# Performance work log

Measured on AMD Instinct MI355X. Metric: run time of the kernel, lower is better.

Reference implementation:

```python
import jax, jax.numpy as jnp
import numpy as np

H = 128          # num_hidden
B = 512          # number of graphs (segments)
N0, N1, N2 = 500_000, 500_000, 250_000  # nodes per rank
EPS = 1e-5       # LayerNorm eps (torch default)


def setup_inputs() -> dict:
    key = jax.random.key(0)
    ks = jax.random.split(key, 24)
    s = 0.02
    inp = {
        "h0": jax.random.normal(ks[0], (N0, H), jnp.float32),
        "h1": jax.random.normal(ks[1], (N1, H), jnp.float32),
        "h2": jax.random.normal(ks[2], (N2, H), jnp.float32),
        "b0": jnp.sort(jax.random.randint(ks[3], (N0,), 0, B, jnp.int32)),
        "b1": jnp.sort(jax.random.randint(ks[4], (N1,), 0, B, jnp.int32)),
        "b2": jnp.sort(jax.random.randint(ks[5], (N2,), 0, B, jnp.int32)),
        "Wg0": jax.random.normal(ks[6], (H, 1), jnp.float32) * s,
        "bg0": jnp.zeros((1,), jnp.float32),
        "Wg1": jax.random.normal(ks[7], (H, 1), jnp.float32) * s,
        "bg1": jnp.zeros((1,), jnp.float32),
        "Wg2": jax.random.normal(ks[8], (H, 1), jnp.float32) * s,
        "bg2": jnp.zeros((1,), jnp.float32),
        "Wp0": jax.random.normal(ks[9], (4 * H, H), jnp.float32) * s,
        "bp0": jnp.zeros((H,), jnp.float32),
        "Wp1": jax.random.normal(ks[10], (4 * H, H), jnp.float32) * s,
        "bp1": jnp.zeros((H,), jnp.float32),
        "Wp2": jax.random.normal(ks[11], (4 * H, H), jnp.float32) * s,
        "bp2": jnp.zeros((H,), jnp.float32),
        "gamma": jnp.ones((3 * H,), jnp.float32),
        "beta": jnp.zeros((3 * H,), jnp.float32),
        "W1": jax.random.normal(ks[12], (3 * H, H), jnp.float32) * s,
        "b1f": jnp.zeros((H,), jnp.float32),
        "W2": jax.random.normal(ks[13], (H, 1), jnp.float32) * s,
        "b2f": jnp.zeros((1,), jnp.float32),
    }
    return inp


def _rank_vec(h, b, Wg, bg, Wp, bp):
    # gated multi-aggregation pooling over segments b -> [B, 4H] -> Linear -> [B, H]
    g = jax.nn.sigmoid(h @ Wg + bg)                      # [N, 1]
    sum_p = jax.ops.segment_sum(h, b, num_segments=B)    # [B, H]
    cnt = jax.ops.segment_sum(jnp.ones((h.shape[0], 1), h.dtype), b, num_segments=B)
    mean_p = sum_p / jnp.maximum(cnt, 1.0)
    max_p = jax.ops.segment_max(h, b, num_segments=B)
    max_p = jnp.where(cnt > 0, max_p, 0.0)               # guard empty segments
    gsum_p = jax.ops.segment_sum(g * h, b, num_segments=B)
    agg = jnp.concatenate([sum_p, mean_p, max_p, gsum_p], axis=1)  # [B, 4H]
    return agg @ Wp + bp


def reference(h0, h1, h2, b0, b1, b2,
              Wg0, bg0, Wg1, bg1, Wg2, bg2,
              Wp0, bp0, Wp1, bp1, Wp2, bp2,
              gamma, beta, W1, b1f, W2, b2f):
    r0 = _rank_vec(h0, b0, Wg0, bg0, Wp0, bp0)
    r1 = _rank_vec(h1, b1, Wg1, bg1, Wp1, bp1)
    r2 = _rank_vec(h2, b2, Wg2, bg2, Wp2, bp2)
    state = jnp.concatenate([r0, r1, r2], axis=1)        # [B, 3H]
    mu = jnp.mean(state, axis=-1, keepdims=True)
    var = jnp.mean(jnp.square(state - mu), axis=-1, keepdims=True)
    xn = (state - mu) * jax.lax.rsqrt(var + EPS) * gamma + beta
    x = jax.nn.silu(xn)
    x = jax.nn.silu(x @ W1 + b1f)
    out = x @ W2 + b2f                                   # [B, 1]
    return out[:, 0] if out.shape[-1] == 1 else out
```

## Files before the change

kernel.cpp:

```cpp
#include <hip/hip_runtime.h>
#include <math.h>

constexpr int H  = 128;
constexpr int B  = 512;
constexpr int RANK_STRIDE = 3 * B * H + B;
constexpr int TOTAL_WS    = 3 * RANK_STRIDE;

constexpr int ROWS_PER_WAVE  = 128;
constexpr int ROWS_PER_BLOCK = 4 * ROWS_PER_WAVE;

__device__ __forceinline__ float atomicMaxF(float* addr, float val) {
  if (val >= 0.f) {
    return __int_as_float(atomicMax((int*)addr, __float_as_int(val)));
  } else {
    return __uint_as_float(atomicMin((unsigned int*)addr, __float_as_uint(val)));
  }
}

__global__ __launch_bounds__(256) void init_ws_kernel(float* ws) {
  int i = blockIdx.x * blockDim.x + threadIdx.x;
  if (i >= TOTAL_WS) return;
  int o = i % RANK_STRIDE;
  bool ismax = (o >= 2 * B * H) && (o < 3 * B * H);
  ws[i] = ismax ? __int_as_float(0xFF800000) : 0.0f;
}

template <int CTRL>
__device__ __forceinline__ float dpp_add(float x) {
  int mi = __builtin_amdgcn_update_dpp(0, __float_as_int(x), CTRL, 0xF, 0xF, true);
  return x + __int_as_float(mi);
}

__global__ __launch_bounds__(256) void rank_fused_kernel(
    const float* __restrict__ h0, const int* __restrict__ b0,
    const float* __restrict__ Wg0, const float* __restrict__ bg0, int N0, int nb0,
    const float* __restrict__ h1, const int* __restrict__ b1,
    const float* __restrict__ Wg1, const float* __restrict__ bg1, int N1, int nb1,
    const float* __restrict__ h2, const int* __restrict__ b2,
    const float* __restrict__ Wg2, const float* __restrict__ bg2, int N2,
    float* __restrict__ ws)
{
  const int blk = blockIdx.x;
  const float* h; const int* b; const float* Wg; const float* bg;
  float* base; int N; int lblk;
  if (blk < nb0) {
    h = h0; b = b0; Wg = Wg0; bg = bg0; base = ws;                   N = N0; lblk = blk;
  } else if (blk < nb0 + nb1) {
    h = h1; b = b1; Wg = Wg1; bg = bg1; base = ws + RANK_STRIDE;     N = N1; lblk = blk - nb0;
  } else {
    h = h2; b = b2; Wg = Wg2; bg = bg2; base = ws + 2 * RANK_STRIDE; N = N2; lblk = blk - nb0 - nb1;
  }

  const int lane = threadIdx.x & 63;
  const int wv   = threadIdx.x >> 6;
  const int half = lane >> 5;
  const int c    = lane & 31;

  const int wstart = (lblk * 4 + wv) * ROWS_PER_WAVE;
  if (wstart >= N) return;
  const int wend = min(wstart + ROWS_PER_WAVE, N);

  float* __restrict__ sumb  = base;
  float* __restrict__ gsumb = base + B * H;
  float* __restrict__ maxb  = base + 2 * B * H;
  float* __restrict__ cntb  = base + 3 * B * H;

  const float4 wg  = ((const float4*)Wg)[c];
  const float  bgv = bg[0];

  const int bv0 = b[min(wstart + lane, N - 1)];
  const int bv1 = b[min(wstart + 64 + lane, N - 1)];

  float4 s  = {0.f, 0.f, 0.f, 0.f};
  float4 gq = {0.f, 0.f, 0.f, 0.f};
  float4 m  = {-INFINITY, -INFINITY, -INFINITY, -INFINITY};
  int cnt = 0;
  int cur = -1;

  auto flushLane = [&]() {
    if (cur >= 0) {
      const int bi = cur * H + c * 4;
      atomicAdd(sumb + bi + 0, s.x);  atomicAdd(sumb + bi + 1, s.y);
      atomicAdd(sumb + bi + 2, s.z);  atomicAdd(sumb + bi + 3, s.w);
      atomicAdd(gsumb + bi + 0, gq.x); atomicAdd(gsumb + bi + 1, gq.y);
      atomicAdd(gsumb + bi + 2, gq.z); atomicAdd(gsumb + bi + 3, gq.w);
      atomicMaxF(maxb + bi + 0, m.x); atomicMaxF(maxb + bi + 1, m.y);
      atomicMaxF(maxb + bi + 2, m.z); atomicMaxF(maxb + bi + 3, m.w);
      if (c == 0 && cnt) atomicAdd(cntb + cur, (float)cnt);
      s = {0.f, 0.f, 0.f, 0.f};
      gq = {0.f, 0.f, 0.f, 0.f};
      m = {-INFINITY, -INFINITY, -INFINITY, -INFINITY};
      cnt = 0;
    }
  };

  auto gateOf = [&](float4 v) -> float {
    float p = fmaf(v.x, wg.x, fmaf(v.y, wg.y, fmaf(v.z, wg.z, v.w * wg.w)));
    p = dpp_add<0xB1>(p);
    p = dpp_add<0x4E>(p);
    p = dpp_add<0x124>(p);
    p = dpp_add<0x128>(p);
    p += __int_as_float(__builtin_amdgcn_ds_swizzle(__float_as_int(p), 0x401F));
    return 1.0f / (1.0f + __expf(-(p + bgv)));
  };

  auto accum = [&](float4 v, float gt) {
    s.x += v.x; s.y += v.y; s.z += v.z; s.w += v.w;
    gq.x = fmaf(gt, v.x, gq.x); gq.y = fmaf(gt, v.y, gq.y);
    gq.z = fmaf(gt, v.z, gq.z); gq.w = fmaf(gt, v.w, gq.w);
    m.x = fmaxf(m.x, v.x); m.y = fmaxf(m.y, v.y);
    m.z = fmaxf(m.z, v.z); m.w = fmaxf(m.w, v.w);
  };

  const float4* __restrict__ hp = (const float4*)h;

  auto LOADB = [&](float4* dst, int baseRow) {
    const float4* rp = hp + (size_t)baseRow * 32 + c;
    #pragma unroll
    for (int i = 0; i < 8; ++i) dst[i] = rp[(size_t)(2 * i + half) * 32];
  };

  float4 cbuf[8];
  bool pre = false;

  int r = wstart;
  while (r + 64 <= wend) {
    const int bv = (r - wstart < 64) ? bv0 : bv1;
    const int sA = __shfl(bv, 0);
    const int sB = __shfl(bv, 63);
    if (sA == sB) {
      if (sA != cur) { flushLane(); cur = sA; }
      if (!pre) LOADB(cbuf, r);
      const bool pnext = (r + 128 <= wend);
      float4 nbuf[8];
      #pragma unroll
      for (int g = 0; g < 4; ++g) {
        if (g < 3) {
          LOADB(nbuf, r + (g + 1) * 16);
        } else if (pnext) {
          LOADB(nbuf, r + 64);
        }
        #pragma unroll
        for (int i = 0; i < 8; ++i) {
          const float gt = gateOf(cbuf[i]);
          accum(cbuf[i], gt);
        }
        #pragma unroll
        for (int i = 0; i < 8; ++i) cbuf[i] = nbuf[i];
      }
      pre = pnext;
      cnt += 32;
    } else {
      #pragma unroll 4
      for (int i = 0; i < 32; ++i) {
        const int seg = __shfl(bv, 2 * i + half);
        const float4 v = hp[(size_t)(r + 2 * i + half) * 32 + c];
        const float gt = gateOf(v);
        if (seg != cur) { flushLane(); cur = seg; }
        accum(v, gt);
        ++cnt;
      }
      pre = false;
    }
    r += 64;
  }
  while (r + 2 <= wend) {
    const int o = r - wstart;
    const int bv = (o < 64) ? bv0 : bv1;
    const int seg = __shfl(bv, (o & 63) + half);
    const float4 v = hp[(size_t)(r + half) * 32 + c];
    const float gt = gateOf(v);
    if (seg != cur) { flushLane(); cur = seg; }
    accum(v, gt);
    ++cnt;
    r += 2;
  }
  if (r < wend) {
    const int o = r - wstart;
    const int bv = (o < 64) ? bv0 : bv1;
    const int seg = __shfl(bv, o & 63);
    const float4 v = hp[(size_t)r * 32 + c];
    const float gt = gateOf(v);
    if (half == 0) {
      if (seg != cur) { flushLane(); cur = seg; }
      accum(v, gt);
      ++cnt;
    }
  }

  {
    const int   ocur = __shfl_xor(cur, 32);
    const float osx = __shfl_xor(s.x, 32), osy = __shfl_xor(s.y, 32);
    const float osz = __shfl_xor(s.z, 32), osw = __shfl_xor(s.w, 32);
    const float ogx = __shfl_xor(gq.x, 32), ogy = __shfl_xor(gq.y, 32);
    const float ogz = __shfl_xor(gq.z, 32), ogw = __shfl_xor(gq.w, 32);
    const float omx = __shfl_xor(m.x, 32), omy = __shfl_xor(m.y, 32);
    const float omz = __shfl_xor(m.z, 32), omw = __shfl_xor(m.w, 32);
    const int   ocnt = __shfl_xor(cnt, 32);
    if (ocur == cur && cur >= 0) {
      if (half == 0) {
        s.x += osx; s.y += osy; s.z += osz; s.w += osw;
        gq.x += ogx; gq.y += ogy; gq.z += ogz; gq.w += ogw;
        m.x = fmaxf(m.x, omx); m.y = fmaxf(m.y, omy);
        m.z = fmaxf(m.z, omz); m.w = fmaxf(m.w, omw);
        cnt += ocnt;
      } else {
        cur = -1;
      }
    }
  }
  flushLane();
}

__device__ __forceinline__ float siluf(float x) {
  return x / (1.0f + __expf(-x));
}

__global__ __launch_bounds__(128) void finalize_kernel(
    const float* __restrict__ ws,
    const float* __restrict__ Wp0, const float* __restrict__ bp0,
    const float* __restrict__ Wp1, const float* __restrict__ bp1,
    const float* __restrict__ Wp2, const float* __restrict__ bp2,
    const float* __restrict__ gamma, const float* __restrict__ beta,
    const float* __restrict__ W1, const float* __restrict__ b1f,
    const float* __restrict__ W2, const float* __restrict__ b2f,
    float* __restrict__ out)
{
  __shared__ float aggL[4][4 * H];
  __shared__ float state[4][3 * H];
  __shared__ float red[8];

  const int j = threadIdx.x;
  const int lane = j & 63;
  const int wv = j >> 6;
  const int gbase = blockIdx.x * 4;

  const float* Wp[3] = {Wp0, Wp1, Wp2};
  const float* bp[3] = {bp0, bp1, bp2};

  for (int k = 0; k < 3; ++k) {
    const float* sumb  = ws + k * RANK_STRIDE;
    const float* gsumb = sumb + B * H;
    const float* maxb  = sumb + 2 * B * H;
    const float* cntb  = sumb + 3 * B * H;

    for (int g = 0; g < 4; ++g) {
      const int bidx = gbase + g;
      const float cc = cntb[bidx];
      const float cm = fmaxf(cc, 1.0f);
      const float sv = sumb[bidx * H + j];
      const float mv = maxb[bidx * H + j];
      const float gv = gsumb[bidx * H + j];
      aggL[g][j]         = sv;
      aggL[g][H + j]     = sv / cm;
      aggL[g][2 * H + j] = (cc > 0.f) ? mv : 0.f;
      aggL[g][3 * H + j] = gv;
    }
    __syncthreads();

    const float bpv = bp[k][j];
    float r0 = bpv, r1 = bpv, r2 = bpv, r3 = bpv;
    const float* W = Wp[k];
    for (int i = 0; i < 4 * H; ++i) {
      const float w = W[i * H + j];
      r0 = fmaf(aggL[0][i], w, r0);
      r1 = fmaf(aggL[1][i], w, r1);
      r2 = fmaf(aggL[2][i], w, r2);
      r3 = fmaf(aggL[3][i], w, r3);
    }
    state[0][k * H + j] = r0;
    state[1][k * H + j] = r1;
    state[2][k * H + j] = r2;
    state[3][k * H + j] = r3;
    __syncthreads();
  }

  for (int g = 0; g < 4; ++g) {
    const float v0 = state[g][j];
    const float v1 = state[g][H + j];
    const float v2 = state[g][2 * H + j];
    float ps = v0 + v1 + v2;
    float pq = v0 * v0 + v1 * v1 + v2 * v2;
    for (int mm = 1; mm < 64; mm <<= 1) {
      ps += __shfl_xor(ps, mm);
      pq += __shfl_xor(pq, mm);
    }
    if (lane == 0) { red[wv * 2] = ps; red[wv * 2 + 1] = pq; }
    __syncthreads();
    const float ts = red[0] + red[2];
    const float tq = red[1] + red[3];
    const float mu  = ts * (1.0f / 384.0f);
    const float var = tq * (1.0f / 384.0f) - mu * mu;
    const float inv = rsqrtf(var + 1e-5f);
    float x0 = (v0 - mu) * inv * gamma[j]         + beta[j];
    float x1 = (v1 - mu) * inv * gamma[H + j]     + beta[H + j];
    float x2 = (v2 - mu) * inv * gamma[2 * H + j] + beta[2 * H + j];
    state[g][j]         = siluf(x0);
    state[g][H + j]     = siluf(x1);
    state[g][2 * H + j] = siluf(x2);
    __syncthreads();
  }

  const float b1v = b1f[j];
  float a0 = b1v, a1 = b1v, a2 = b1v, a3 = b1v;
  for (int i = 0; i < 3 * H; ++i) {
    const float w = W1[i * H + j];
    a0 = fmaf(state[0][i], w, a0);
    a1 = fmaf(state[1][i], w, a1);
    a2 = fmaf(state[2][i], w, a2);
    a3 = fmaf(state[3][i], w, a3);
  }
  a0 = siluf(a0); a1 = siluf(a1); a2 = siluf(a2); a3 = siluf(a3);

  const float w2 = W2[j];
  float p0 = a0 * w2, p1 = a1 * w2, p2 = a2 * w2, p3 = a3 * w2;
  for (int mm = 1; mm < 64; mm <<= 1) {
    p0 += __shfl_xor(p0, mm);
    p1 += __shfl_xor(p1, mm);
    p2 += __shfl_xor(p2, mm);
    p3 += __shfl_xor(p3, mm);
  }
  __syncthreads();
  if (lane == 0) {
    red[wv * 4 + 0] = p0; red[wv * 4 + 1] = p1;
    red[wv * 4 + 2] = p2; red[wv * 4 + 3] = p3;
  }
  __syncthreads();
  if (j < 4) out[gbase + j] = red[j] + red[4 + j] + b2f[0];
}

extern "C" void kernel_launch(void* const* d_in, const int* in_sizes, int n_in,
                              void* d_out, int out_size, void* d_ws, size_t ws_size,
                              hipStream_t stream) {
  const float* h0  = (const float*)d_in[0];
  const float* h1  = (const float*)d_in[1];
  const float* h2  = (const float*)d_in[2];
  const int*   b0  = (const int*)d_in[3];
  const int*   b1  = (const int*)d_in[4];
  const int*   b2  = (const int*)d_in[5];
  const float* Wg0 = (const float*)d_in[6];
  const float* bg0 = (const float*)d_in[7];
  const float* Wg1 = (const float*)d_in[8];
  const float* bg1 = (const float*)d_in[9];
  const float* Wg2 = (const float*)d_in[10];
  const float* bg2 = (const float*)d_in[11];
  const float* Wp0 = (const float*)d_in[12];
  const float* bp0 = (const float*)d_in[13];
  const float* Wp1 = (const float*)d_in[14];
  const float* bp1 = (const float*)d_in[15];
  const float* Wp2 = (const float*)d_in[16];
  const float* bp2 = (const float*)d_in[17];
  const float* gamma = (const float*)d_in[18];
  const float* beta  = (const float*)d_in[19];
  const float* W1  = (const float*)d_in[20];
  const float* b1f = (const float*)d_in[21];
  const float* W2  = (const float*)d_in[22];
  const float* b2f = (const float*)d_in[23];

  const int N0 = in_sizes[3];
  const int N1 = in_sizes[4];
  const int N2 = in_sizes[5];

  float* ws = (float*)d_ws;

  {
    int blocks = (TOTAL_WS + 255) / 256;
    hipLaunchKernelGGL(init_ws_kernel, dim3(blocks), dim3(256), 0, stream, ws);
  }

  const int nb0 = (N0 + ROWS_PER_BLOCK - 1) / ROWS_PER_BLOCK;
  const int nb1 = (N1 + ROWS_PER_BLOCK - 1) / ROWS_PER_BLOCK;
  const int nb2 = (N2 + ROWS_PER_BLOCK - 1) / ROWS_PER_BLOCK;
  hipLaunchKernelGGL(rank_fused_kernel, dim3(nb0 + nb1 + nb2), dim3(256), 0, stream,
                     h0, b0, Wg0, bg0, N0, nb0,
                     h1, b1, Wg1, bg1, N1, nb1,
                     h2, b2, Wg2, bg2, N2,
                     ws);

  hipLaunchKernelGGL(finalize_kernel, dim3(B / 4), dim3(128), 0, stream,
                     ws, Wp0, bp0, Wp1, bp1, Wp2, bp2,
                     gamma, beta, W1, b1f, W2, b2f, (float*)d_out);
}
```

Baseline: 736.1 us.

## Merge per-wave segment partials in LDS before global atomics; restructure prefetch

Each half-wave's final partial (sum, gated sum, max, count) is written to shared memory, and one warp merges partials that share a segment before issuing global atomics. This cuts global atomic traffic, which is high because sorted segments span many waves. The uniform-segment path also moves from an 8-row batched prefetch to a 2-row ping-pong double buffer, and launch bounds now request 8 blocks per CU. The costs are an added block barrier and a serial merge done by a single warp.

After: 1.043 ms. 1.42x slower.

```diff
diff --git a/kernel.cpp b/kernel.cpp
--- a/kernel.cpp
+++ b/kernel.cpp
@@ -31,7 +31,7 @@
   return x + __int_as_float(mi);
 }
 
-__global__ __launch_bounds__(256) void rank_fused_kernel(
+__global__ __launch_bounds__(256, 8) void rank_fused_kernel(
     const float* __restrict__ h0, const int* __restrict__ b0,
     const float* __restrict__ Wg0, const float* __restrict__ bg0, int N0, int nb0,
     const float* __restrict__ h1, const int* __restrict__ b1,
@@ -40,6 +40,10 @@
     const float* __restrict__ Wg2, const float* __restrict__ bg2, int N2,
     float* __restrict__ ws)
 {
+  __shared__ float lsP[8][32][12];
+  __shared__ int   lsSeg[8];
+  __shared__ float lsCnt[8];
+
   const int blk = blockIdx.x;
   const float* h; const int* b; const float* Wg; const float* bg;
   float* base; int N; int lblk;
@@ -57,7 +61,7 @@
   const int c    = lane & 31;
 
   const int wstart = (lblk * 4 + wv) * ROWS_PER_WAVE;
-  if (wstart >= N) return;
+  const bool active = (wstart < N);
   const int wend = min(wstart + ROWS_PER_WAVE, N);
 
   float* __restrict__ sumb  = base;
@@ -114,102 +118,156 @@
 
   const float4* __restrict__ hp = (const float4*)h;
 
-  auto LOADB = [&](float4* dst, int baseRow) {
-    const float4* rp = hp + (size_t)baseRow * 32 + c;
-    #pragma unroll
-    for (int i = 0; i < 8; ++i) dst[i] = rp[(size_t)(2 * i + half) * 32];
+  auto LOAD2 = [&](float4& d0, float4& d1, int baseRow) {
+    const float4* rp = hp + (size_t)(baseRow + half) * 32 + c;
+    d0 = rp[0];
+    d1 = rp[64];
   };
-
-  float4 cbuf[8];
-  bool pre = false;
-
-  int r = wstart;
-  while (r + 64 <= wend) {
-    const int bv = (r - wstart < 64) ? bv0 : bv1;
-    const int sA = __shfl(bv, 0);
-    const int sB = __shfl(bv, 63);
-    if (sA == sB) {
-      if (sA != cur) { flushLane(); cur = sA; }
-      if (!pre) LOADB(cbuf, r);
-      const bool pnext = (r + 128 <= wend);
-      float4 nbuf[8];
-      #pragma unroll
-      for (int g = 0; g < 4; ++g) {
-        if (g < 3) {
-          LOADB(nbuf, r + (g + 1) * 16);
-        } else if (pnext) {
-          LOADB(nbuf, r + 64);
+  auto COMP2 = [&](const float4& v0, const float4& v1) {
+    { const float gt = gateOf(v0); accum(v0, gt); }
+    { const float gt = gateOf(v1); accum(v1, gt); }
+  };
+
+  if (active) {
+    float4 A0, A1;
+    float4 B0, B1;
+    bool preA = false;
+
+    int r = wstart;
+    while (r + 64 <= wend) {
+      const int bv = (r - wstart < 64) ? bv0 : bv1;
+      const int sA = __shfl(bv, 0);
+      const int sB = __shfl(bv, 63);
+      if (sA == sB) {
+        if (sA != cur) { flushLane(); cur = sA; }
+        if (!preA) LOAD2(A0, A1, r);
+        LOAD2(B0, B1, r +  4);  COMP2(A0, A1);
+        LOAD2(A0, A1, r +  8);  COMP2(B0, B1);
+        LOAD2(B0, B1, r + 12);  COMP2(A0, A1);
+        LOAD2(A0, A1, r + 16);  COMP2(B0, B1);
+        LOAD2(B0, B1, r + 20);  COMP2(A0, A1);
+        LOAD2(A0, A1, r + 24);  COMP2(B0, B1);
+        LOAD2(B0, B1, r + 28);  COMP2(A0, A1);
+        LOAD2(A0, A1, r + 32);  COMP2(B0, B1);
+        LOAD2(B0, B1, r + 36);  COMP2(A0, A1);
+        LOAD2(A0, A1, r + 40);  COMP2(B0, B1);
+        LOAD2(B0, B1, r + 44);  COMP2(A0, A1);
+        LOAD2(A0, A1, r + 48);  COMP2(B0, B1);
+        LOAD2(B0, B1, r + 52);  COMP2(A0, A1);
+        LOAD2(A0, A1, r + 56);  COMP2(B0, B1);
+        LOAD2(B0, B1, r + 60);  COMP2(A0, A1);
+        const bool pnext = (r + 128 <= wend);
+        if (pnext) LOAD2(A0, A1, r + 64);
+        COMP2(B0, B1);
+        preA = pnext;
+        cnt += 32;
+      } else {
+        #pragma unroll 4
+        for (int i = 0; i < 32; ++i) {
+          const int seg = __shfl(bv, 2 * i + half);
+          const float4 v = hp[(size_t)(r + 2 * i + half) * 32 + c];
+          const float gt = gateOf(v);
+          if (seg != cur) { flushLane(); cur = seg; }
+          accum(v, gt);
+          ++cnt;
         }
-        #pragma unroll
-        for (int i = 0; i < 8; ++i) {
-          const float gt = gateOf(cbuf[i]);
-          accum(cbuf[i], gt);
-        }
-        #pragma unroll
-        for (int i = 0; i < 8; ++i) cbuf[i] = nbuf[i];
+        preA = false;
       }
-      pre = pnext;
-      cnt += 32;
-    } else {
-      #pragma unroll 4
-      for (int i = 0; i < 32; ++i) {
-        const int seg = __shfl(bv, 2 * i + half);
-        const float4 v = hp[(size_t)(r + 2 * i + half) * 32 + c];
-        const float gt = gateOf(v);
+      r += 64;
+    }
+    while (r + 2 <= wend) {
+      const int o = r - wstart;
+      const int bv = (o < 64) ? bv0 : bv1;
+      const int seg = __shfl(bv, (o & 63) + half);
+      const float4 v = hp[(size_t)(r + half) * 32 + c];
+      const float gt = gateOf(v);
+      if (seg != cur) { flushLane(); cur = seg; }
+      accum(v, gt);
+      ++cnt;
+      r += 2;
+    }
+    if (r < wend) {
+      const int o = r - wstart;
+      const int bv = (o < 64) ? bv0 : bv1;
+      const int seg = __shfl(bv, o & 63);
+      const float4 v = hp[(size_t)r * 32 + c];
+      const float gt = gateOf(v);
+      if (half == 0) {
         if (seg != cur) { flushLane(); cur = seg; }
         accum(v, gt);
         ++cnt;
       }
-      pre = false;
-    }
-    r += 64;
-  }
-  while (r + 2 <= wend) {
-    const int o = r - wstart;
-    const int bv = (o < 64) ? bv0 : bv1;
-    const int seg = __shfl(bv, (o & 63) + half);
-    const float4 v = hp[(size_t)(r + half) * 32 + c];
-    const float gt = gateOf(v);
-    if (seg != cur) { flushLane(); cur = seg; }
-    accum(v, gt);
-    ++cnt;
-    r += 2;
-  }
-  if (r < wend) {
-    const int o = r - wstart;
-    const int bv = (o < 64) ? bv0 : bv1;
-    const int seg = __shfl(bv, o & 63);
-    const float4 v = hp[(size_t)r * 32 + c];
-    const float gt = gateOf(v);
-    if (half == 0) {
-      if (seg != cur) { flushLane(); cur = seg; }
-      accum(v, gt);
-      ++cnt;
+    }
+
+    {
+      const int   ocur = __shfl_xor(cur, 32);
+      const float osx = __shfl_xor(s.x, 32), osy = __shfl_xor(s.y, 32);
+      const float osz = __shfl_xor(s.z, 32), osw = __shfl_xor(s.w, 32);
+      const float ogx = __shfl_xor(gq.x, 32), ogy = __shfl_xor(gq.y, 32);
+      const float ogz = __shfl_xor(gq.z, 32), ogw = __shfl_xor(gq.w, 32);
+      const float omx = __shfl_xor(m.x, 32), omy = __shfl_xor(m.y, 32);
+      const float omz = __shfl_xor(m.z, 32), omw = __shfl_xor(m.w, 32);
+      const int   ocnt = __shfl_xor(cnt, 32);
+      if (ocur == cur && cur >= 0) {
+        if (half == 0) {
+          s.x += osx; s.y += osy; s.z += osz; s.w += osw;
+          gq.x += ogx; gq.y += ogy; gq.z += ogz; gq.w += ogw;
+          m.x = fmaxf(m.x, omx); m.y = fmaxf(m.y, omy);
+          m.z = fmaxf(m.z, omz); m.w = fmaxf(m.w, omw);
+          cnt += ocnt;
+        } else {
+          cur = -1;
+        }
+      }
     }
   }
 
   {
-    const int   ocur = __shfl_xor(cur, 32);
-    const float osx = __shfl_xor(s.x, 32), osy = __shfl_xor(s.y, 32);
-    const float osz = __shfl_xor(s.z, 32), osw = __shfl_xor(s.w, 32);
-    const float ogx = __shfl_xor(gq.x, 32), ogy = __shfl_xor(gq.y, 32);
-    const float ogz = __shfl_xor(gq.z, 32), ogw = __shfl_xor(gq.w, 32);
-    const float omx = __shfl_xor(m.x, 32), omy = __shfl_xor(m.y, 32);
-    const float omz = __shfl_xor(m.z, 32), omw = __shfl_xor(m.w, 32);
-    const int   ocnt = __shfl_xor(cnt, 32);
-    if (ocur == cur && cur >= 0) {
-      if (half == 0) {
-        s.x += osx; s.y += osy; s.z += osz; s.w += osw;
-        gq.x += ogx; gq.y += ogy; gq.z += ogz; gq.w += ogw;
-        m.x = fmaxf(m.x, omx); m.y = fmaxf(m.y, omy);
-        m.z = fmaxf(m.z, omz); m.w = fmaxf(m.w, omw);
-        cnt += ocnt;
-      } else {
-        cur = -1;
+    const int slot = wv * 2 + half;
+    float* dst = &lsP[slot][c][0];
+    *(float4*)(dst + 0) = s;
+    *(float4*)(dst + 4) = gq;
+    *(float4*)(dst + 8) = m;
+    if (c == 0) { lsSeg[slot] = cur; lsCnt[slot] = (float)cnt; }
+  }
+  __syncthreads();
+  if (threadIdx.x < 32) {
+    const int l = threadIdx.x;
+    int   seg[8]; float cn[8];
+    #pragma unroll
+    for (int p = 0; p < 8; ++p) { seg[p] = lsSeg[p]; cn[p] = lsCnt[p]; }
+    unsigned done = 0;
+    #pragma unroll
+    for (int p = 0; p < 8; ++p) {
+      if (seg[p] < 0 || ((done >> p) & 1)) continue;
+      float4 S = *(float4*)&lsP[p][l][0];
+      float4 G = *(float4*)&lsP[p][l][4];
+      float4 M = *(float4*)&lsP[p][l][8];
+      float  C = cn[p];
+      #pragma unroll
+      for (int q = p + 1; q < 8; ++q) {
+        if (seg[q] == seg[p]) {
+          done |= 1u << q;
+          const float4 S2 = *(float4*)&lsP[q][l][0];
+          const float4 G2 = *(float4*)&lsP[q][l][4];
+          const float4 M2 = *(float4*)&lsP[q][l][8];
+          S.x += S2.x; S.y += S2.y; S.z += S2.z; S.w += S2.w;
+          G.x += G2.x; G.y += G2.y; G.z += G2.z; G.w += G2.w;
+          M.x = fmaxf(M.x, M2.x); M.y = fmaxf(M.y, M2.y);
+          M.z = fmaxf(M.z, M2.z); M.w = fmaxf(M.w, M2.w);
+          C += cn[q];
+        }
       }
-    }
-  }
-  flushLane();
+      const int bi = seg[p] * H + l * 4;
+      atomicAdd(sumb + bi + 0, S.x);  atomicAdd(sumb + bi + 1, S.y);
+      atomicAdd(sumb + bi + 2, S.z);  atomicAdd(sumb + bi + 3, S.w);
+      atomicAdd(gsumb + bi + 0, G.x); atomicAdd(gsumb + bi + 1, G.y);
+      atomicAdd(gsumb + bi + 2, G.z); atomicAdd(gsumb + bi + 3, G.w);
+      atomicMaxF(maxb + bi + 0, M.x); atomicMaxF(maxb + bi + 1, M.y);
+      atomicMaxF(maxb + bi + 2, M.z); atomicMaxF(maxb + bi + 3, M.w);
+      if (l == 0 && C > 0.f) atomicAdd(cntb + seg[p], C);
+    }
+  }
 }
 
 __device__ __forceinline__ float siluf(float x) {
```
